# Performance work log

Measured on AMD Instinct MI355X. Metric: run time of the kernel, lower is better.

## Reference

```python
import jax, jax.numpy as jnp
import numpy as np

ENC_H = 128
DEC_H = 256
DEC_STEPS = 10


def _gru_cell(x, h, Wih, Whh, bih, bhh):
    # PyTorch GRU cell, gate order (r, z, n)
    gi = x @ Wih.T + bih          # (B, 3H)
    gh = h @ Whh.T + bhh          # (B, 3H)
    H = h.shape[-1]
    ir, iz, inn = gi[:, :H], gi[:, H:2 * H], gi[:, 2 * H:]
    hr, hz, hn = gh[:, :H], gh[:, H:2 * H], gh[:, 2 * H:]
    r = jax.nn.sigmoid(ir + hr)
    z = jax.nn.sigmoid(iz + hz)
    n = jnp.tanh(inn + r * hn)
    return (1.0 - z) * n + z * h


def setup_inputs() -> dict:
    key = jax.random.key(0)
    ks = jax.random.split(key, 12)
    B, S = 4096, 128
    s = 0.1
    return {
        "x": jax.random.normal(ks[0], (B, S, 5), jnp.float32),
        "y": jax.random.normal(ks[1], (B, S, 1), jnp.float32),
        "enc_Wih": jax.random.normal(ks[2], (3 * ENC_H, 5), jnp.float32) * s,
        "enc_Whh": jax.random.normal(ks[3], (3 * ENC_H, ENC_H), jnp.float32) * s,
        "enc_bih": jax.random.normal(ks[4], (3 * ENC_H,), jnp.float32) * s,
        "enc_bhh": jax.random.normal(ks[5], (3 * ENC_H,), jnp.float32) * s,
        "dec_Wih": jax.random.normal(ks[6], (3 * DEC_H, ENC_H + 1), jnp.float32) * s,
        "dec_Whh": jax.random.normal(ks[7], (3 * DEC_H, DEC_H), jnp.float32) * s,
        "dec_bih": jax.random.normal(ks[8], (3 * DEC_H,), jnp.float32) * s,
        "dec_bhh": jax.random.normal(ks[9], (3 * DEC_H,), jnp.float32) * s,
        "lin_W": jax.random.normal(ks[10], (4, DEC_H), jnp.float32) * s,
        "lin_b": jax.random.normal(ks[11], (4,), jnp.float32) * s,
    }


def reference(x, y, enc_Wih, enc_Whh, enc_bih, enc_bhh,
              dec_Wih, dec_Whh, dec_bih, dec_bhh, lin_W, lin_b):
    B, S, _ = x.shape
    xs = jnp.transpose(x, (1, 0, 2))   # (S, B, 5)
    ys = jnp.transpose(y, (1, 0, 2))   # (S, B, 1)

    # Encoder: only the final hidden state (contex) is consumed downstream.
    h0 = jnp.zeros((B, ENC_H), x.dtype)

    def enc_step(h, xt):
        return _gru_cell(xt, h, enc_Wih, enc_Whh, enc_bih, enc_bhh), None

    contex, _ = jax.lax.scan(enc_step, h0, xs)   # (B, 128)

    # Decoder: initial hidden is ones (torch.ones_like(shape)), 10 steps.
    hdec0 = jnp.ones((B, DEC_H), x.dtype)

    def dec_step(h, yt):
        xt = jnp.concatenate([contex, yt], axis=-1)   # (B, 129)
        h2 = _gru_cell(xt, h, dec_Wih, dec_Whh, dec_bih, dec_bhh)
        out = h2 @ lin_W.T + lin_b                    # (B, 4)
        return h2, out

    _, outs = jax.lax.scan(dec_step, hdec0, ys[:DEC_STEPS])  # (10, B, 4)

    # res starts as ones; only first 10 rows written.
    res = jnp.ones((S, B, 4), x.dtype).at[:DEC_STEPS].set(outs)
    return jnp.transpose(res, (1, 0, 2))   # (B, S, 4)
```

## Files before the change

kernel.cpp:

```cpp
#include <hip/hip_runtime.h>

#define B_SZ 4096
#define S_SZ 128
#define XD 5
#define EH 128
#define DH 256
#define DSTEPS 10

typedef short v8s __attribute__((ext_vector_type(8)));
typedef float v4f __attribute__((ext_vector_type(4)));

__device__ __forceinline__ float bf2f(unsigned short u) {
    union { unsigned int i; float f; } v; v.i = ((unsigned int)u) << 16; return v.f;
}
__device__ __forceinline__ unsigned short f2bf(float f) {
    union { float f; unsigned int i; } v; v.f = f;
    unsigned int x = v.i;
    return (unsigned short)((x + 0x7FFFu + ((x >> 16) & 1u)) >> 16);
}
__device__ __forceinline__ float fexp2(float x) { return __builtin_amdgcn_exp2f(x); }
__device__ __forceinline__ float frcp(float x) { return __builtin_amdgcn_rcpf(x); }
__device__ __forceinline__ unsigned int cvt2bf(float lo, float hi) {
    unsigned int r;
    asm("v_cvt_pk_bf16_f32 %0, %1, %2" : "=v"(r) : "v"(lo), "v"(hi));
    return r;
}

#define SC_S (-1.44269504088896f)
#define SC_T ( 2.88539008177793f)

__global__ __launch_bounds__(512) void enc_kernel(
    const float* __restrict__ x,
    const float* __restrict__ Wih32,
    const float* __restrict__ Whh32,
    const float* __restrict__ bih,
    const float* __restrict__ bhh,
    const float* __restrict__ dWih,
    const float* __restrict__ dWhh,
    unsigned short* __restrict__ wihp,
    unsigned short* __restrict__ dWhh_bf,
    unsigned short* __restrict__ ctex)
{
    __shared__ unsigned short xs[S_SZ][16][8];
    __shared__ unsigned short hb[2][16][136];
    __shared__ __align__(16) unsigned short zpad[8];

    const int tid = threadIdx.x;
    const int bid = blockIdx.x;
    const int wv = tid >> 6;
    const int lane = tid & 63;
    const int n = lane & 15;
    const int kg = lane >> 4;
    const int r0 = bid * 16;

    for (int i = bid * 512 + tid; i < 768 * 256; i += 131072) {
        const float sc = ((i >> 8) < 512) ? SC_S : SC_T;
        dWhh_bf[i] = f2bf(sc * dWhh[i]);
    }
    for (int i = bid * 512 + tid; i < 768 * 136; i += 131072) {
        int col = i / 136, k = i - col * 136;
        const float sc = (col < 512) ? SC_S : SC_T;
        wihp[i] = (k < 129) ? f2bf(sc * dWih[col * 129 + k]) : (unsigned short)0;
    }

    for (int i = tid; i < 2 * 16 * 136; i += 512) ((unsigned short*)hb)[i] = 0;
    if (tid < 8) zpad[tid] = 0;
    for (int i = tid; i < 16 * S_SZ * 8; i += 512) {
        int m = i >> 10;
        int rem = i & 1023;
        int t = rem >> 3;
        int j = rem & 7;
        unsigned short v = 0;
        if (j < XD) v = f2bf(x[(size_t)(r0 + m) * (S_SZ * XD) + t * XD + j]);
        else if (j == XD) v = 0x3F80;
        xs[t][m][j] = v;
    }

    const int colw = wv * 16 + n;
    v8s fw[3][4];
    v8s fx[3];
    #pragma unroll
    for (int g = 0; g < 3; ++g) {
        const float sc = (g < 2) ? SC_S : SC_T;
        const int gcol = g * EH + colw;
        #pragma unroll
        for (int kt = 0; kt < 4; ++kt) {
            const float* p = &Whh32[(size_t)gcol * EH + kt * 32 + kg * 8];
            float4 lo = *(const float4*)p;
            float4 hi = *(const float4*)(p + 4);
            v8s f;
            f[0] = (short)f2bf(sc * lo.x); f[1] = (short)f2bf(sc * lo.y);
            f[2] = (short)f2bf(sc * lo.z); f[3] = (short)f2bf(sc * lo.w);
            f[4] = (short)f2bf(sc * hi.x); f[5] = (short)f2bf(sc * hi.y);
            f[6] = (short)f2bf(sc * hi.z); f[7] = (short)f2bf(sc * hi.w);
            fw[g][kt] = f;
        }
        v8s t = {0, 0, 0, 0, 0, 0, 0, 0};
        if (kg == 0) {
            const float* p = &Wih32[gcol * XD];
            #pragma unroll
            for (int j = 0; j < XD; ++j) t[j] = (short)f2bf(sc * p[j]);
            float b = (g < 2) ? (sc * (bih[gcol] + bhh[gcol]))
                              : (sc * bih[gcol]);
            t[XD] = (short)f2bf(b);
        }
        fx[g] = t;
    }
    const float bhn = SC_T * bhh[2 * EH + colw];

    const v4f vzero = {0.f, 0.f, 0.f, 0.f};
    float hst[4] = {0.f, 0.f, 0.f, 0.f};
    __syncthreads();

    #pragma unroll 2
    for (int t = 0; t < S_SZ; ++t) {
        const int p = t & 1;
        v8s a[4];
        #pragma unroll
        for (int kt = 0; kt < 4; ++kt)
            a[kt] = *(const v8s*)&hb[p][n][kt * 32 + kg * 8];
        const unsigned short* xsrc = (kg == 0) ? &xs[t][n][0] : &zpad[0];
        v8s ax = *(const v8s*)xsrc;

        v4f accr  = __builtin_amdgcn_mfma_f32_16x16x32_bf16(a[0], fw[0][0], vzero, 0, 0, 0);
        v4f accz  = __builtin_amdgcn_mfma_f32_16x16x32_bf16(a[0], fw[1][0], vzero, 0, 0, 0);
        v4f acchn = __builtin_amdgcn_mfma_f32_16x16x32_bf16(a[0], fw[2][0], vzero, 0, 0, 0);
        #pragma unroll
        for (int kt = 1; kt < 4; ++kt) {
            accr  = __builtin_amdgcn_mfma_f32_16x16x32_bf16(a[kt], fw[0][kt], accr, 0, 0, 0);
            accz  = __builtin_amdgcn_mfma_f32_16x16x32_bf16(a[kt], fw[1][kt], accz, 0, 0, 0);
            acchn = __builtin_amdgcn_mfma_f32_16x16x32_bf16(a[kt], fw[2][kt], acchn, 0, 0, 0);
        }
        accr = __builtin_amdgcn_mfma_f32_16x16x32_bf16(ax, fx[0], accr, 0, 0, 0);
        accz = __builtin_amdgcn_mfma_f32_16x16x32_bf16(ax, fx[1], accz, 0, 0, 0);
        v4f accin = __builtin_amdgcn_mfma_f32_16x16x32_bf16(ax, fx[2], vzero, 0, 0, 0);

        float hnew[4];
        #pragma unroll
        for (int e = 0; e < 4; ++e) {
            float r  = frcp(1.f + fexp2(accr[e]));
            float z  = frcp(1.f + fexp2(accz[e]));
            float nn = 1.f - 2.f * frcp(fexp2(accin[e] + r * (acchn[e] + bhn)) + 1.f);
            float h  = nn + z * (hst[e] - nn);
            hst[e] = h;
            hnew[e] = h;
        }
        const unsigned int pk01 = cvt2bf(hnew[0], hnew[1]);
        const unsigned int pk23 = cvt2bf(hnew[2], hnew[3]);
        hb[1 - p][kg * 4 + 0][colw] = (unsigned short)(pk01 & 0xFFFFu);
        hb[1 - p][kg * 4 + 1][colw] = (unsigned short)(pk01 >> 16);
        hb[1 - p][kg * 4 + 2][colw] = (unsigned short)(pk23 & 0xFFFFu);
        hb[1 - p][kg * 4 + 3][colw] = (unsigned short)(pk23 >> 16);
        __syncthreads();
    }
    #pragma unroll
    for (int e = 0; e < 4; ++e)
        ctex[(size_t)(r0 + kg * 4 + e) * EH + colw] = f2bf(hst[e]);
}

__global__ __launch_bounds__(512)
__attribute__((amdgpu_waves_per_eu(2, 2)))
void dec_all_kernel(
    const unsigned short* __restrict__ dWhh_bf,
    const unsigned short* __restrict__ wihp,
    const float* __restrict__ dbih,
    const float* __restrict__ dbhh,
    const float* __restrict__ y,
    const unsigned short* __restrict__ ctex,
    const float* __restrict__ linW,
    const float* __restrict__ linb,
    float* __restrict__ out)
{
    __shared__ unsigned short wshn[32 * 258 * 8];
    __shared__ unsigned short hshf[32 * 16 * 8];
    __shared__ unsigned short lwf[32 * 16 * 8];
    __shared__ float ysh[16][DSTEPS];

    const int tid  = threadIdx.x;
    const int w    = tid >> 6;
    const int lane = tid & 63;
    const int n    = lane & 15;
    const int kg   = lane >> 4;
    const int rb   = blockIdx.x * 16;
    const int cbase = w * 32;

    for (int i = tid; i < 256 * 32; i += 512) {
        int col = i >> 5, kgrp = i & 31;
        uint4 v = *(const uint4*)&dWhh_bf[(size_t)(512 + col) * 256 + kgrp * 8];
        *(uint4*)&wshn[(kgrp * 258 + col) * 8] = v;
    }
    {
        int col = tid >> 5, kgrp = tid & 31;
        unsigned short v8[8];
        #pragma unroll
        for (int j = 0; j < 8; ++j)
            v8[j] = (col < 4) ? f2bf(linW[col * 256 + kgrp * 8 + j]) : (unsigned short)0;
        *(uint4*)&lwf[(kgrp * 16 + col) * 8] = *(uint4*)v8;
    }
    if (tid < 16 * DSTEPS) {
        int row = tid / DSTEPS, tt = tid - row * DSTEPS;
        ysh[row][tt] = y[(size_t)(rb + row) * S_SZ + tt];
    }
    for (int i = tid; i < 32 * 16 * 8; i += 512) hshf[i] = 0x3F80;

    v8s fB[2][2][8];
    #pragma unroll
    for (int g = 0; g < 2; ++g)
        #pragma unroll
        for (int cg = 0; cg < 2; ++cg)
            #pragma unroll
            for (int kt = 0; kt < 8; ++kt)
                fB[g][cg][kt] = *(const v8s*)
                    &dWhh_bf[(size_t)(g * DH + cbase + cg * 16 + n) * DH + kt * 32 + kg * 8];

    v4f gi[3][2];
    float wy[3][2], bNh[2];
    #pragma unroll
    for (int g = 0; g < 3; ++g)
        #pragma unroll
        for (int cg = 0; cg < 2; ++cg) {
            int gcol = g * DH + cbase + cg * 16 + n;
            const float sc = (g < 2) ? SC_S : SC_T;
            float bb = sc * (dbih[gcol] + ((g < 2) ? dbhh[gcol] : 0.f));
            gi[g][cg] = (v4f){bb, bb, bb, bb};
            wy[g][cg] = bf2f(wihp[(size_t)gcol * 136 + 128]);
        }
    #pragma unroll
    for (int cg = 0; cg < 2; ++cg)
        bNh[cg] = SC_T * dbhh[2 * DH + cbase + cg * 16 + n];

    #pragma unroll
    for (int kt = 0; kt < 4; ++kt) {
        v8s a = *(const v8s*)&ctex[(size_t)(rb + n) * EH + kt * 32 + kg * 8];
        #pragma unroll
        for (int g = 0; g < 3; ++g)
            #pragma unroll
            for (int cg = 0; cg < 2; ++cg) {
                v8s b = *(const v8s*)
                    &wihp[(size_t)(g * DH + cbase + cg * 16 + n) * 136 + kt * 32 + kg * 8];
                gi[g][cg] = __builtin_amdgcn_mfma_f32_16x16x32_bf16(a, b, gi[g][cg], 0, 0, 0);
            }
    }

    const float lb = (n < 4) ? linb[n] : 0.f;
    float hprev[2][4];
    #pragma unroll
    for (int cg = 0; cg < 2; ++cg)
        #pragma unroll
        for (int e = 0; e < 4; ++e) hprev[cg][e] = 1.0f;

    __syncthreads();

    for (int t = 0; t < DSTEPS; ++t) {
        float yv[4];
        #pragma unroll
        for (int e = 0; e < 4; ++e)
            yv[e] = ysh[kg * 4 + e][t];

        v4f ar[2], az[2], an[2];
        #pragma unroll
        for (int cg = 0; cg < 2; ++cg) {
            ar[cg] = (v4f){0.f, 0.f, 0.f, 0.f};
            az[cg] = (v4f){0.f, 0.f, 0.f, 0.f};
            an[cg] = (v4f){bNh[cg], bNh[cg], bNh[cg], bNh[cg]};
        }
        #pragma unroll
        for (int kt = 0; kt < 8; ++kt) {
            v8s a = *(const v8s*)&hshf[((kt * 4 + kg) * 16 + n) * 8];
            #pragma unroll
            for (int cg = 0; cg < 2; ++cg) {
                v8s bn_ = *(const v8s*)&wshn[((kt * 4 + kg) * 258 + cbase + cg * 16 + n) * 8];
                ar[cg] = __builtin_amdgcn_mfma_f32_16x16x32_bf16(a, fB[0][cg][kt], ar[cg], 0, 0, 0);
                az[cg] = __builtin_amdgcn_mfma_f32_16x16x32_bf16(a, fB[1][cg][kt], az[cg], 0, 0, 0);
                an[cg] = __builtin_amdgcn_mfma_f32_16x16x32_bf16(a, bn_,           an[cg], 0, 0, 0);
            }
        }
        __syncthreads();

        #pragma unroll
        for (int cg = 0; cg < 2; ++cg) {
            const int chi = 4 * w + 2 * cg + (n >> 3);
            #pragma unroll
            for (int e = 0; e < 4; ++e) {
                float r  = frcp(1.f + fexp2(gi[0][cg][e] + yv[e] * wy[0][cg] + ar[cg][e]));
                float z  = frcp(1.f + fexp2(gi[1][cg][e] + yv[e] * wy[1][cg] + az[cg][e]));
                float nn = 1.f - 2.f * frcp(
                    fexp2(gi[2][cg][e] + yv[e] * wy[2][cg] + r * an[cg][e]) + 1.f);
                float h  = nn + z * (hprev[cg][e] - nn);
                hprev[cg][e] = h;
                hshf[(chi * 16 + kg * 4 + e) * 8 + (n & 7)] = f2bf(h);
            }
        }
        __syncthreads();

        if (w == 0) {
            v4f o4 = {0.f, 0.f, 0.f, 0.f};
            #pragma unroll
            for (int kt = 0; kt < 8; ++kt) {
                v8s a = *(const v8s*)&hshf[((kt * 4 + kg) * 16 + n) * 8];
                v8s b = *(const v8s*)&lwf[((kt * 4 + kg) * 16 + n) * 8];
                o4 = __builtin_amdgcn_mfma_f32_16x16x32_bf16(a, b, o4, 0, 0, 0);
            }
            if (n < 4) {
                #pragma unroll
                for (int e = 0; e < 4; ++e)
                    out[(size_t)(rb + kg * 4 + e) * (S_SZ * 4) + t * 4 + n] = o4[e] + lb;
            }
        }
    }

    for (int j = tid; j < 16 * 512; j += 512) {
        int row = j >> 9, c = j & 511;
        if (c >= DSTEPS * 4) out[(size_t)(rb + row) * 512 + c] = 1.0f;
    }
}

extern "C" void kernel_launch(void* const* d_in, const int* in_sizes, int n_in,
                              void* d_out, int out_size, void* d_ws, size_t ws_size,
                              hipStream_t stream)
{
    const float* x    = (const float*)d_in[0];
    const float* y    = (const float*)d_in[1];
    const float* eWih = (const float*)d_in[2];
    const float* eWhh = (const float*)d_in[3];
    const float* ebih = (const float*)d_in[4];
    const float* ebhh = (const float*)d_in[5];
    const float* dWih = (const float*)d_in[6];
    const float* dWhh = (const float*)d_in[7];
    const float* dbih = (const float*)d_in[8];
    const float* dbhh = (const float*)d_in[9];
    const float* linW = (const float*)d_in[10];
    const float* linb = (const float*)d_in[11];
    float* out = (float*)d_out;

    char* ws = (char*)d_ws;
    unsigned short* wihp    = (unsigned short*)(ws);
    unsigned short* dWhh_bf = (unsigned short*)(ws + 208896);
    unsigned short* ctex    = (unsigned short*)(ws + 602112);

    enc_kernel<<<256, 512, 0, stream>>>(x, eWih, eWhh, ebih, ebhh,
                                        dWih, dWhh, wihp, dWhh_bf, ctex);
    dec_all_kernel<<<256, 512, 0, stream>>>(dWhh_bf, wihp, dbih, dbhh, y,
                                            ctex, linW, linb, out);
}
```

Before: 203.2 us.

## Keep all decoder Whh gates in registers and transpose MFMA operand roles

```diff
diff --git a/kernel.cpp b/kernel.cpp
--- a/kernel.cpp
+++ b/kernel.cpp
@@ -171,9 +171,10 @@
     const float* __restrict__ linb,
     float* __restrict__ out)
 {
-    __shared__ unsigned short wshn[32 * 258 * 8];
     __shared__ unsigned short hshf[32 * 16 * 8];
     __shared__ unsigned short lwf[32 * 16 * 8];
+    __shared__ float gish[512 * 28];
+    __shared__ float wysh[512 * 28];
     __shared__ float ysh[16][DSTEPS];
 
     const int tid  = threadIdx.x;
@@ -184,11 +185,6 @@
     const int rb   = blockIdx.x * 16;
     const int cbase = w * 32;
 
-    for (int i = tid; i < 256 * 32; i += 512) {
-        int col = i >> 5, kgrp = i & 31;
-        uint4 v = *(const uint4*)&dWhh_bf[(size_t)(512 + col) * 256 + kgrp * 8];
-        *(uint4*)&wshn[(kgrp * 258 + col) * 8] = v;
-    }
     {
         int col = tid >> 5, kgrp = tid & 31;
         unsigned short v8[8];
@@ -203,9 +199,9 @@
     }
     for (int i = tid; i < 32 * 16 * 8; i += 512) hshf[i] = 0x3F80;
 
-    v8s fB[2][2][8];
-    #pragma unroll
-    for (int g = 0; g < 2; ++g)
+    v8s fB[3][2][8];
+    #pragma unroll
+    for (int g = 0; g < 3; ++g)
         #pragma unroll
         for (int cg = 0; cg < 2; ++cg)
             #pragma unroll
@@ -213,98 +209,120 @@
                 fB[g][cg][kt] = *(const v8s*)
                     &dWhh_bf[(size_t)(g * DH + cbase + cg * 16 + n) * DH + kt * 32 + kg * 8];
 
+    const v4f vzero = {0.f, 0.f, 0.f, 0.f};
     v4f gi[3][2];
-    float wy[3][2], bNh[2];
     #pragma unroll
     for (int g = 0; g < 3; ++g)
         #pragma unroll
+        for (int cg = 0; cg < 2; ++cg) gi[g][cg] = vzero;
+
+    #pragma unroll
+    for (int kt = 0; kt < 4; ++kt) {
+        v8s actex = *(const v8s*)&ctex[(size_t)(rb + n) * EH + kt * 32 + kg * 8];
+        #pragma unroll
+        for (int g = 0; g < 3; ++g)
+            #pragma unroll
+            for (int cg = 0; cg < 2; ++cg) {
+                v8s bw = *(const v8s*)
+                    &wihp[(size_t)(g * DH + cbase + cg * 16 + n) * 136 + kt * 32 + kg * 8];
+                gi[g][cg] = __builtin_amdgcn_mfma_f32_16x16x32_bf16(bw, actex, gi[g][cg], 0, 0, 0);
+            }
+    }
+
+    #pragma unroll
+    for (int g = 0; g < 3; ++g) {
+        const float sc = (g < 2) ? SC_S : SC_T;
+        #pragma unroll
         for (int cg = 0; cg < 2; ++cg) {
-            int gcol = g * DH + cbase + cg * 16 + n;
-            const float sc = (g < 2) ? SC_S : SC_T;
-            float bb = sc * (dbih[gcol] + ((g < 2) ? dbhh[gcol] : 0.f));
-            gi[g][cg] = (v4f){bb, bb, bb, bb};
-            wy[g][cg] = bf2f(wihp[(size_t)gcol * 136 + 128]);
-        }
+            #pragma unroll
+            for (int e = 0; e < 4; ++e) {
+                const int col = cbase + cg * 16 + kg * 4 + e;
+                const int gcol = g * DH + col;
+                float bb = sc * (dbih[gcol] + ((g < 2) ? dbhh[gcol] : 0.f));
+                gi[g][cg][e] += bb;
+                wysh[tid * 28 + (g * 2 + cg) * 4 + e] = bf2f(wihp[(size_t)gcol * 136 + 128]);
+            }
+        }
+    }
+    #pragma unroll
+    for (int g = 0; g < 3; ++g)
+        #pragma unroll
+        for (int cg = 0; cg < 2; ++cg)
+            *(v4f*)&gish[tid * 28 + (g * 2 + cg) * 4] = gi[g][cg];
+    #pragma unroll
+    for (int e = 0; e < 4; ++e) {
+        gish[tid * 28 + 24 + e] = SC_T * dbhh[2 * DH + cbase + 0 * 16 + kg * 4 + e];
+        wysh[tid * 28 + 24 + e] = SC_T * dbhh[2 * DH + cbase + 1 * 16 + kg * 4 + e];
+    }
+
+    const float4 lb4 = *(const float4*)linb;
+    float hprev[2][4];
     #pragma unroll
     for (int cg = 0; cg < 2; ++cg)
-        bNh[cg] = SC_T * dbhh[2 * DH + cbase + cg * 16 + n];
-
-    #pragma unroll
-    for (int kt = 0; kt < 4; ++kt) {
-        v8s a = *(const v8s*)&ctex[(size_t)(rb + n) * EH + kt * 32 + kg * 8];
-        #pragma unroll
-        for (int g = 0; g < 3; ++g)
-            #pragma unroll
-            for (int cg = 0; cg < 2; ++cg) {
-                v8s b = *(const v8s*)
-                    &wihp[(size_t)(g * DH + cbase + cg * 16 + n) * 136 + kt * 32 + kg * 8];
-                gi[g][cg] = __builtin_amdgcn_mfma_f32_16x16x32_bf16(a, b, gi[g][cg], 0, 0, 0);
-            }
-    }
-
-    const float lb = (n < 4) ? linb[n] : 0.f;
-    float hprev[2][4];
-    #pragma unroll
-    for (int cg = 0; cg < 2; ++cg)
         #pragma unroll
         for (int e = 0; e < 4; ++e) hprev[cg][e] = 1.0f;
 
     __syncthreads();
 
     for (int t = 0; t < DSTEPS; ++t) {
-        float yv[4];
-        #pragma unroll
-        for (int e = 0; e < 4; ++e)
-            yv[e] = ysh[kg * 4 + e][t];
+        const float yv = ysh[n][t];
 
         v4f ar[2], az[2], an[2];
         #pragma unroll
-        for (int cg = 0; cg < 2; ++cg) {
-            ar[cg] = (v4f){0.f, 0.f, 0.f, 0.f};
-            az[cg] = (v4f){0.f, 0.f, 0.f, 0.f};
-            an[cg] = (v4f){bNh[cg], bNh[cg], bNh[cg], bNh[cg]};
-        }
+        for (int cg = 0; cg < 2; ++cg) { ar[cg] = vzero; az[cg] = vzero; an[cg] = vzero; }
+
         #pragma unroll
         for (int kt = 0; kt < 8; ++kt) {
             v8s a = *(const v8s*)&hshf[((kt * 4 + kg) * 16 + n) * 8];
             #pragma unroll
             for (int cg = 0; cg < 2; ++cg) {
-                v8s bn_ = *(const v8s*)&wshn[((kt * 4 + kg) * 258 + cbase + cg * 16 + n) * 8];
-                ar[cg] = __builtin_amdgcn_mfma_f32_16x16x32_bf16(a, fB[0][cg][kt], ar[cg], 0, 0, 0);
-                az[cg] = __builtin_amdgcn_mfma_f32_16x16x32_bf16(a, fB[1][cg][kt], az[cg], 0, 0, 0);
-                an[cg] = __builtin_amdgcn_mfma_f32_16x16x32_bf16(a, bn_,           an[cg], 0, 0, 0);
+                ar[cg] = __builtin_amdgcn_mfma_f32_16x16x32_bf16(fB[0][cg][kt], a, ar[cg], 0, 0, 0);
+                az[cg] = __builtin_amdgcn_mfma_f32_16x16x32_bf16(fB[1][cg][kt], a, az[cg], 0, 0, 0);
+                an[cg] = __builtin_amdgcn_mfma_f32_16x16x32_bf16(fB[2][cg][kt], a, an[cg], 0, 0, 0);
             }
         }
         __syncthreads();
 
         #pragma unroll
         for (int cg = 0; cg < 2; ++cg) {
-            const int chi = 4 * w + 2 * cg + (n >> 3);
+            v4f giR = *(const v4f*)&gish[tid * 28 + (0 * 2 + cg) * 4];
+            v4f giZ = *(const v4f*)&gish[tid * 28 + (1 * 2 + cg) * 4];
+            v4f giN = *(const v4f*)&gish[tid * 28 + (2 * 2 + cg) * 4];
+            v4f wyR = *(const v4f*)&wysh[tid * 28 + (0 * 2 + cg) * 4];
+            v4f wyZ = *(const v4f*)&wysh[tid * 28 + (1 * 2 + cg) * 4];
+            v4f wyN = *(const v4f*)&wysh[tid * 28 + (2 * 2 + cg) * 4];
+            v4f bN  = (cg == 0) ? *(const v4f*)&gish[tid * 28 + 24]
+                                : *(const v4f*)&wysh[tid * 28 + 24];
+            float hh[4];
             #pragma unroll
             for (int e = 0; e < 4; ++e) {
-                float r  = frcp(1.f + fexp2(gi[0][cg][e] + yv[e] * wy[0][cg] + ar[cg][e]));
-                float z  = frcp(1.f + fexp2(gi[1][cg][e] + yv[e] * wy[1][cg] + az[cg][e]));
+                float r  = frcp(1.f + fexp2(giR[e] + yv * wyR[e] + ar[cg][e]));
+                float z  = frcp(1.f + fexp2(giZ[e] + yv * wyZ[e] + az[cg][e]));
                 float nn = 1.f - 2.f * frcp(
-                    fexp2(gi[2][cg][e] + yv[e] * wy[2][cg] + r * an[cg][e]) + 1.f);
+                    fexp2(giN[e] + yv * wyN[e] + r * (an[cg][e] + bN[e])) + 1.f);
                 float h  = nn + z * (hprev[cg][e] - nn);
                 hprev[cg][e] = h;
-                hshf[(chi * 16 + kg * 4 + e) * 8 + (n & 7)] = f2bf(h);
-            }
+                hh[e] = h;
+            }
+            const unsigned int p01 = cvt2bf(hh[0], hh[1]);
+            const unsigned int p23 = cvt2bf(hh[2], hh[3]);
+            const int base = cbase + cg * 16 + kg * 4;
+            const int idx = (((base >> 3) * 16) + n) * 8 + (base & 7);
+            *(uint2*)&hshf[idx] = (uint2){p01, p23};
         }
         __syncthreads();
 
-        if (w == 0) {
-            v4f o4 = {0.f, 0.f, 0.f, 0.f};
+        if (w == (t & 7)) {
+            v4f o4 = vzero;
             #pragma unroll
             for (int kt = 0; kt < 8; ++kt) {
                 v8s a = *(const v8s*)&hshf[((kt * 4 + kg) * 16 + n) * 8];
                 v8s b = *(const v8s*)&lwf[((kt * 4 + kg) * 16 + n) * 8];
-                o4 = __builtin_amdgcn_mfma_f32_16x16x32_bf16(a, b, o4, 0, 0, 0);
-            }
-            if (n < 4) {
-                #pragma unroll
-                for (int e = 0; e < 4; ++e)
-                    out[(size_t)(rb + kg * 4 + e) * (S_SZ * 4) + t * 4 + n] = o4[e] + lb;
+                o4 = __builtin_amdgcn_mfma_f32_16x16x32_bf16(b, a, o4, 0, 0, 0);
+            }
+            if (kg == 0) {
+                float4 ov = {o4[0] + lb4.x, o4[1] + lb4.y, o4[2] + lb4.z, o4[3] + lb4.w};
+                *(float4*)&out[(size_t)(rb + n) * (S_SZ * 4) + t * 4] = ov;
             }
         }
     }
```

Result: slower. 219.7 us (+8.1%).
